# Kernel tuning notes

Hardware: AMD Instinct MI355X
Metric: run time of the kernel (lower is better)

The kernel has to match this reference:

```python
import jax, jax.numpy as jnp
import numpy as np

# Model/config constants (match init_kwargs)
B, S, D, H = 2, 2048, 512, 8
HD = D // H            # head dim = 64
WIN, DIL, G = 16, 2, 64  # window size, dilation rate, num global tokens
L = S - G              # 1984 local tokens (global indices are 0..G-1)


def setup_inputs() -> dict:
    key = jax.random.key(0)
    ks = jax.random.split(key, 16)
    sc = 0.02
    n = jax.random.normal
    return {
        "query": n(ks[0], (B, S, D), jnp.float32),
        "key": n(ks[1], (B, S, D), jnp.float32),
        "value": n(ks[2], (B, S, D), jnp.float32),
        # local multi-head attention params (linear_query/key/value/out_proj)
        "wq": n(ks[3], (D, D), jnp.float32) * sc, "bq": jnp.zeros((D,), jnp.float32),
        "wk": n(ks[4], (D, D), jnp.float32) * sc, "bk": jnp.zeros((D,), jnp.float32),
        "wv": n(ks[5], (D, D), jnp.float32) * sc, "bv": jnp.zeros((D,), jnp.float32),
        "wo": n(ks[6], (D, D), jnp.float32) * sc, "bo": jnp.zeros((D,), jnp.float32),
        # global nn.MultiheadAttention params (packed in_proj + out_proj)
        "g_in_w": n(ks[7], (3 * D, D), jnp.float32) * sc,
        "g_in_b": jnp.zeros((3 * D,), jnp.float32),
        "g_out_w": n(ks[8], (D, D), jnp.float32) * sc,
        "g_out_b": jnp.zeros((D,), jnp.float32),
    }


def _window_indices():
    # centered dilated window per local position, clipped to valid range
    pos = jnp.arange(L)
    offs = DIL * (jnp.arange(WIN) - WIN // 2)
    return jnp.clip(pos[:, None] + offs[None, :], 0, L - 1)


def reference(query, key, value, wq, bq, wk, bk, wv, bv, wo, bo,
              g_in_w, g_in_b, g_out_w, g_out_b):
    scale = 1.0 / np.sqrt(HD).astype(np.float32)

    # ---- local (dilated sliding window) path over tokens G..S-1 ----
    q_loc = query[:, G:, :]                      # (B, L, D)
    widx = _window_indices()
    k_win = key[:, G:, :][:, widx, :]
    v_win = value[:, G:, :][:, widx, :]

    q = (q_loc @ wq.T + bq).reshape(B, L, H, HD)          # (B,L,H,HD)
    k = (k_win @ wk.T + bk).reshape(B, L, WIN, H, HD)     # (B,L,W,H,HD)
    v = (v_win @ wv.T + bv).reshape(B, L, WIN, H, HD)

    scores = jnp.einsum('blhd,blwhd->blhw', q, k) * scale
    p = jax.nn.softmax(scores, axis=-1)
    o = jnp.einsum('blhw,blwhd->blhd', p, v).reshape(B, L, D)
    local_out = o @ wo.T + bo                              # (B,L,D)

    # ---- global token path: standard MHA over the G global tokens ----
    wq_g, wk_g, wv_g = g_in_w[:D], g_in_w[D:2 * D], g_in_w[2 * D:]
    bq_g, bk_g, bv_g = g_in_b[:D], g_in_b[D:2 * D], g_in_b[2 * D:]
    qg = (query[:, :G] @ wq_g.T + bq_g).reshape(B, G, H, HD)
    kg = (key[:, :G] @ wk_g.T + bk_g).reshape(B, G, H, HD)
    vg = (value[:, :G] @ wv_g.T + bv_g).reshape(B, G, H, HD)
    sg = jnp.einsum('bqhd,bkhd->bhqk', qg, kg) * scale     # (B,H,G,G)
    pg = jax.nn.softmax(sg, axis=-1)
    og = jnp.einsum('bhqk,bkhd->bqhd', pg, vg).reshape(B, G, D)
    global_out = og @ g_out_w.T + g_out_b                  # (B,G,D)

    # ---- fuse: scatter local + global back into full sequence ----
    out = jnp.zeros((B, S, D), query.dtype)
    out = out.at[:, G:, :].set(local_out)
    out = out.at[:, :G, :].set(global_out)
    return out
```

## Files before the change

### kernel.cpp

```cpp
#include <hip/hip_runtime.h>
#include <stdint.h>

#define B_ 2
#define S_ 2048
#define D_ 512
#define H_ 8
#define WIN_ 16
#define DIL_ 2
#define G_ 64
#define L_ (S_ - G_)

typedef short bf16x8 __attribute__((ext_vector_type(8)));
typedef float f32x4 __attribute__((ext_vector_type(4)));
typedef unsigned short u16;

__device__ __forceinline__ float bf2f(u16 h) {
  return __uint_as_float(((uint32_t)h) << 16);
}
__device__ __forceinline__ u16 f2bf(float f) {
  uint32_t u = __float_as_uint(f);
  uint32_t r = (u + 0x7fffu + ((u >> 16) & 1u)) >> 16;
  return (u16)r;
}

__device__ __forceinline__ void gload16(const u16* g, u16* l) {
  __builtin_amdgcn_global_load_lds(
      (const __attribute__((address_space(1))) void*)g,
      (__attribute__((address_space(3))) void*)l, 16, 0, 0);
}

struct CvtJob { const float* src; u16* dst; int n4; };
struct CvtArgs { CvtJob job[9]; };

__global__ __launch_bounds__(256) void cvt_kernel(CvtArgs a) {
  CvtJob j = a.job[blockIdx.y];
  int stride = gridDim.x * blockDim.x;
  for (int i = blockIdx.x * blockDim.x + threadIdx.x; i < j.n4; i += stride) {
    float4 v = reinterpret_cast<const float4*>(j.src)[i];
    ushort4 o;
    o.x = f2bf(v.x); o.y = f2bf(v.y); o.z = f2bf(v.z); o.w = f2bf(v.w);
    reinterpret_cast<ushort4*>(j.dst)[i] = o;
  }
}

struct Job {
  const u16* X; const u16* W; const float* bias; void* Y;
  int rpb;
  int xoff;
  long xbs;
  int yoff;
  long ybs;
  int out_f32;
};
struct GemmLaunch { int start[6]; Job job[6]; };

__global__ __launch_bounds__(256) void gemm_kernel(GemmLaunch a) {
  int bid = (int)blockIdx.x;
  bid = (bid & 7) * ((int)gridDim.x >> 3) + (bid >> 3);

  int j = 0;
#pragma unroll
  for (int i = 1; i < 6; ++i) j = (bid >= a.start[i]) ? i : j;
  const Job jb = a.job[j];
  bid -= a.start[j];
  const int tm = bid >> 2, tn = bid & 3;
  const int row0 = tm * 128, n0 = tn * 128;

  __shared__ __align__(16) u16 As[2][128 * 32];
  __shared__ __align__(16) u16 Bs[2][128 * 32];

  const int tid = threadIdx.x, lane = tid & 63, w = tid >> 6;
  const int wm = w >> 1, wn = w & 1;

  const int rA = tid >> 2;
  const int kq = (tid & 3) * 8;

  const int r0 = row0 + rA,      b0 = r0 >= jb.rpb;
  const int r1 = row0 + 64 + rA, b1 = r1 >= jb.rpb;
  const u16* xa0 = jb.X + (size_t)(b0 ? jb.xbs : 0) +
                   (size_t)(jb.xoff + r0 - (b0 ? jb.rpb : 0)) * 512 + kq;
  const u16* xa1 = jb.X + (size_t)(b1 ? jb.xbs : 0) +
                   (size_t)(jb.xoff + r1 - (b1 ? jb.rpb : 0)) * 512 + kq;
  const u16* wb0 = jb.W + (size_t)(n0 + rA) * 512 + kq;
  const u16* wb1 = jb.W + (size_t)(n0 + 64 + rA) * 512 + kq;

  f32x4 acc[4][4];
#pragma unroll
  for (int i = 0; i < 4; ++i)
#pragma unroll
    for (int k = 0; k < 4; ++k) acc[i][k] = (f32x4){0.f, 0.f, 0.f, 0.f};

  auto stage = [&](int buf, int kof) {
    gload16(xa0 + kof, &As[buf][w * 512]);
    gload16(xa1 + kof, &As[buf][2048 + w * 512]);
    gload16(wb0 + kof, &Bs[buf][w * 512]);
    gload16(wb1 + kof, &Bs[buf][2048 + w * 512]);
  };
  auto compute = [&](int buf) {
    bf16x8 af[4], bfv[4];
#pragma unroll
    for (int fm = 0; fm < 4; ++fm)
      af[fm] = *(const bf16x8*)&As[buf][(wm * 64 + fm * 16 + (lane & 15)) * 32 + 8 * (lane >> 4)];
#pragma unroll
    for (int fn = 0; fn < 4; ++fn)
      bfv[fn] = *(const bf16x8*)&Bs[buf][(wn * 64 + fn * 16 + (lane & 15)) * 32 + 8 * (lane >> 4)];
#pragma unroll
    for (int fm = 0; fm < 4; ++fm)
#pragma unroll
      for (int fn = 0; fn < 4; ++fn)
        acc[fm][fn] = __builtin_amdgcn_mfma_f32_16x16x32_bf16(af[fm], bfv[fn], acc[fm][fn], 0, 0, 0);
  };

  stage(0, 0);
  __syncthreads();
  int cur = 0;
  for (int kt = 0; kt < 15; ++kt) {
    stage(cur ^ 1, (kt + 1) * 32);
    compute(cur);
    __syncthreads();
    cur ^= 1;
  }
  compute(cur);

#pragma unroll
  for (int fm = 0; fm < 4; ++fm) {
#pragma unroll
    for (int fn = 0; fn < 4; ++fn) {
#pragma unroll
      for (int r = 0; r < 4; ++r) {
        const int row = row0 + wm * 64 + fm * 16 + (lane >> 4) * 4 + r;
        const int col = n0 + wn * 64 + fn * 16 + (lane & 15);
        const int b = row >= jb.rpb;
        const int rr = row - (b ? jb.rpb : 0);
        const size_t yi = (size_t)(b ? jb.ybs : 0) + (size_t)(jb.yoff + rr) * 512 + col;
        const float v = acc[fm][fn][r] + jb.bias[col];
        if (jb.out_f32) ((float*)jb.Y)[yi] = v;
        else            ((u16*)jb.Y)[yi]   = f2bf(v);
      }
    }
  }
}

__global__ __launch_bounds__(256) void attn_kernel(const u16* qp, const u16* kp,
                                                   const u16* vp, u16* ob,
                                                   const u16* qgp, const u16* kgp,
                                                   const u16* vgp, u16* ogp) {
  const int lane = threadIdx.x & 63;
  int bid = (int)blockIdx.x;
  const int nbl = (B_ * L_) / 4;
  if (bid < nbl) bid = (bid & 7) * (nbl >> 3) + (bid >> 3);
  const int wid = bid * 4 + (threadIdx.x >> 6);

  if (wid < B_ * L_) {
    const int l = wid % L_;
    const int brow = wid - l;
    float q[8];
    {
      bf16x8 qv = *(const bf16x8*)&qp[(size_t)wid * 512 + lane * 8];
#pragma unroll
      for (int e = 0; e < 8; ++e) q[e] = bf2f((u16)qv[e]);
    }
    float s[WIN_];
#pragma unroll
    for (int w2 = 0; w2 < WIN_; ++w2) {
      int ki = l + DIL_ * w2 - WIN_;
      ki = ki < 0 ? 0 : (ki > L_ - 1 ? L_ - 1 : ki);
      bf16x8 kv = *(const bf16x8*)&kp[(size_t)(brow + ki) * 512 + lane * 8];
      float p = 0.f;
#pragma unroll
      for (int e = 0; e < 8; ++e) p = fmaf(q[e], bf2f((u16)kv[e]), p);
      p += __shfl_xor(p, 1); p += __shfl_xor(p, 2); p += __shfl_xor(p, 4);
      s[w2] = p * 0.125f;
    }
    float m = s[0];
#pragma unroll
    for (int w2 = 1; w2 < WIN_; ++w2) m = fmaxf(m, s[w2]);
    float sum = 0.f;
#pragma unroll
    for (int w2 = 0; w2 < WIN_; ++w2) { s[w2] = __expf(s[w2] - m); sum += s[w2]; }
    const float inv = 1.0f / sum;
    float acc[8] = {0.f};
#pragma unroll
    for (int w2 = 0; w2 < WIN_; ++w2) {
      int ki = l + DIL_ * w2 - WIN_;
      ki = ki < 0 ? 0 : (ki > L_ - 1 ? L_ - 1 : ki);
      bf16x8 vv = *(const bf16x8*)&vp[(size_t)(brow + ki) * 512 + lane * 8];
#pragma unroll
      for (int e = 0; e < 8; ++e) acc[e] = fmaf(s[w2], bf2f((u16)vv[e]), acc[e]);
    }
    bf16x8 o8;
#pragma unroll
    for (int e = 0; e < 8; ++e) o8[e] = (short)f2bf(acc[e] * inv);
    *(bf16x8*)&ob[(size_t)wid * 512 + lane * 8] = o8;
  } else {
    const int g = wid - B_ * L_;
    const int base = (g >> 6) * 64;
    const int qi = g & 63;
    float q[8];
    {
      bf16x8 qv = *(const bf16x8*)&qgp[(size_t)(base + qi) * 512 + lane * 8];
#pragma unroll
      for (int e = 0; e < 8; ++e) q[e] = bf2f((u16)qv[e]);
    }
    float m = -1e30f, sum = 0.f, acc[8] = {0.f};
    for (int j2 = 0; j2 < 64; ++j2) {
      bf16x8 kv = *(const bf16x8*)&kgp[(size_t)(base + j2) * 512 + lane * 8];
      float p = 0.f;
#pragma unroll
      for (int e = 0; e < 8; ++e) p = fmaf(q[e], bf2f((u16)kv[e]), p);
      p += __shfl_xor(p, 1); p += __shfl_xor(p, 2); p += __shfl_xor(p, 4);
      p *= 0.125f;
      const float mn = fmaxf(m, p);
      const float c  = __expf(m - mn);
      const float pe = __expf(p - mn);
      sum = sum * c + pe;
      m = mn;
      bf16x8 vv = *(const bf16x8*)&vgp[(size_t)(base + j2) * 512 + lane * 8];
#pragma unroll
      for (int e = 0; e < 8; ++e) acc[e] = acc[e] * c + pe * bf2f((u16)vv[e]);
    }
    const float inv = 1.0f / sum;
    bf16x8 o8;
#pragma unroll
    for (int e = 0; e < 8; ++e) o8[e] = (short)f2bf(acc[e] * inv);
    *(bf16x8*)&ogp[(size_t)(base + qi) * 512 + lane * 8] = o8;
  }
}

extern "C" void kernel_launch(void* const* d_in, const int* in_sizes, int n_in,
                              void* d_out, int out_size, void* d_ws, size_t ws_size,
                              hipStream_t stream) {
  const float* query   = (const float*)d_in[0];
  const float* key     = (const float*)d_in[1];
  const float* value   = (const float*)d_in[2];
  const float* wq      = (const float*)d_in[3];
  const float* bq      = (const float*)d_in[4];
  const float* wk      = (const float*)d_in[5];
  const float* bk      = (const float*)d_in[6];
  const float* wv      = (const float*)d_in[7];
  const float* bv      = (const float*)d_in[8];
  const float* wo      = (const float*)d_in[9];
  const float* bo      = (const float*)d_in[10];
  const float* g_in_w  = (const float*)d_in[11];
  const float* g_in_b  = (const float*)d_in[12];
  const float* g_out_w = (const float*)d_in[13];
  const float* g_out_b = (const float*)d_in[14];
  float* out = (float*)d_out;

  u16* w16 = (u16*)d_ws;
  const size_t QKV = (size_t)B_ * S_ * D_;
  const size_t WSZ = (size_t)D_ * D_;
  const size_t PSZ = (size_t)B_ * L_ * D_;
  const size_t GSZ = (size_t)B_ * G_ * D_;

  u16* qb  = w16;              u16* kb  = qb + QKV;   u16* vb  = kb + QKV;
  u16* wqb = vb + QKV;         u16* wkb = wqb + WSZ;  u16* wvb = wkb + WSZ;
  u16* wob = wvb + WSZ;
  u16* gqw = wob + WSZ;        u16* gkw = gqw + WSZ;  u16* gvw = gkw + WSZ;
  u16* gow = gvw + WSZ;
  u16* qp  = gow + WSZ;        u16* kp  = qp + PSZ;   u16* vp  = kp + PSZ;
  u16* ob  = vp + PSZ;
  u16* qgp = ob + PSZ;         u16* kgp = qgp + GSZ;  u16* vgp = kgp + GSZ;
  u16* ogp = vgp + GSZ;

  CvtArgs ca;
  ca.job[0] = {query, qb, (int)(QKV / 4)};
  ca.job[1] = {key,   kb, (int)(QKV / 4)};
  ca.job[2] = {value, vb, (int)(QKV / 4)};
  ca.job[3] = {wq, wqb, (int)(WSZ / 4)};
  ca.job[4] = {wk, wkb, (int)(WSZ / 4)};
  ca.job[5] = {wv, wvb, (int)(WSZ / 4)};
  ca.job[6] = {wo, wob, (int)(WSZ / 4)};
  ca.job[7] = {g_in_w, gqw, (int)(3 * WSZ / 4)};
  ca.job[8] = {g_out_w, gow, (int)(WSZ / 4)};
  hipLaunchKernelGGL(cvt_kernel, dim3(512, 9), dim3(256), 0, stream, ca);

  const long XBS = (long)S_ * D_;
  const long PBS = (long)L_ * D_;
  const long GBS = (long)G_ * D_;

  GemmLaunch gi;
  gi.start[0] = 0; gi.start[1] = 124; gi.start[2] = 248;
  gi.start[3] = 372; gi.start[4] = 376; gi.start[5] = 380;
  gi.job[0] = {qb, wqb, bq, qp, L_, G_, XBS, 0, PBS, 0};
  gi.job[1] = {kb, wkb, bk, kp, L_, G_, XBS, 0, PBS, 0};
  gi.job[2] = {vb, wvb, bv, vp, L_, G_, XBS, 0, PBS, 0};
  gi.job[3] = {qb, gqw, g_in_b,           qgp, G_, 0, XBS, 0, GBS, 0};
  gi.job[4] = {kb, gkw, g_in_b + D_,      kgp, G_, 0, XBS, 0, GBS, 0};
  gi.job[5] = {vb, gvw, g_in_b + 2 * D_,  vgp, G_, 0, XBS, 0, GBS, 0};
  hipLaunchKernelGGL(gemm_kernel, dim3(384), dim3(256), 0, stream, gi);

  hipLaunchKernelGGL(attn_kernel, dim3((B_ * L_ + 128) / 4), dim3(256), 0, stream,
                     qp, kp, vp, ob, qgp, kgp, vgp, ogp);

  GemmLaunch go;
  go.start[0] = 0; go.start[1] = 124;
  go.start[2] = go.start[3] = go.start[4] = go.start[5] = 0x7fffffff;
  go.job[0] = {ob,  wob, bo,      out, L_, 0, PBS, G_, XBS, 1};
  go.job[1] = {ogp, gow, g_out_b, out, G_, 0, GBS, 0,  XBS, 1};
  go.job[2] = go.job[1]; go.job[3] = go.job[1]; go.job[4] = go.job[1]; go.job[5] = go.job[1];
  hipLaunchKernelGGL(gemm_kernel, dim3(128), dim3(256), 0, stream, go);
}
```

Measured before the change: 181.6 us.

## Fuse fp32-to-bf16 conversion into GEMM staging and drop separate convert kernel

Removes the standalone cvt_kernel, which converted all inputs and weights to bf16 in a separate pass. The GEMM now reads fp32 activations and weights directly, converts them in registers and stores bf16 to padded LDS. The padding (row stride 36) is meant to reduce bank conflicts. The tile changes to 128x64 to double the block count, and the async global_load_lds path is replaced by synchronous register loads, which costs memory-latency hiding and makes each weight tile be reconverted by many blocks.

```diff
diff --git a/kernel.cpp b/kernel.cpp
--- a/kernel.cpp
+++ b/kernel.cpp
@@ -14,6 +14,8 @@
 typedef float f32x4 __attribute__((ext_vector_type(4)));
 typedef unsigned short u16;
 
+#define LDSW 36
+
 __device__ __forceinline__ float bf2f(u16 h) {
   return __uint_as_float(((uint32_t)h) << 16);
 }
@@ -22,29 +24,12 @@
   uint32_t r = (u + 0x7fffu + ((u >> 16) & 1u)) >> 16;
   return (u16)r;
 }
-
-__device__ __forceinline__ void gload16(const u16* g, u16* l) {
-  __builtin_amdgcn_global_load_lds(
-      (const __attribute__((address_space(1))) void*)g,
-      (__attribute__((address_space(3))) void*)l, 16, 0, 0);
-}
-
-struct CvtJob { const float* src; u16* dst; int n4; };
-struct CvtArgs { CvtJob job[9]; };
-
-__global__ __launch_bounds__(256) void cvt_kernel(CvtArgs a) {
-  CvtJob j = a.job[blockIdx.y];
-  int stride = gridDim.x * blockDim.x;
-  for (int i = blockIdx.x * blockDim.x + threadIdx.x; i < j.n4; i += stride) {
-    float4 v = reinterpret_cast<const float4*>(j.src)[i];
-    ushort4 o;
-    o.x = f2bf(v.x); o.y = f2bf(v.y); o.z = f2bf(v.z); o.w = f2bf(v.w);
-    reinterpret_cast<ushort4*>(j.dst)[i] = o;
-  }
+__device__ __forceinline__ uint32_t pack2(float lo, float hi) {
+  return (uint32_t)f2bf(lo) | ((uint32_t)f2bf(hi) << 16);
 }
 
 struct Job {
-  const u16* X; const u16* W; const float* bias; void* Y;
+  const void* X; const float* W; const float* bias; void* Y;
   int rpb;
   int xoff;
   long xbs;
@@ -54,6 +39,7 @@
 };
 struct GemmLaunch { int start[6]; Job job[6]; };
 
+template <int X_BF16>
 __global__ __launch_bounds__(256) void gemm_kernel(GemmLaunch a) {
   int bid = (int)blockIdx.x;
   bid = (bid & 7) * ((int)gridDim.x >> 3) + (bid >> 3);
@@ -63,51 +49,66 @@
   for (int i = 1; i < 6; ++i) j = (bid >= a.start[i]) ? i : j;
   const Job jb = a.job[j];
   bid -= a.start[j];
-  const int tm = bid >> 2, tn = bid & 3;
-  const int row0 = tm * 128, n0 = tn * 128;
-
-  __shared__ __align__(16) u16 As[2][128 * 32];
-  __shared__ __align__(16) u16 Bs[2][128 * 32];
+  const int tm = bid >> 3, tn = bid & 7;
+  const int row0 = tm * 128, n0 = tn * 64;
+
+  __shared__ __align__(16) u16 As[2][128 * LDSW];
+  __shared__ __align__(16) u16 Bs[2][64 * LDSW];
 
   const int tid = threadIdx.x, lane = tid & 63, w = tid >> 6;
   const int wm = w >> 1, wn = w & 1;
 
-  const int rA = tid >> 2;
+  const int rs = tid >> 2;
   const int kq = (tid & 3) * 8;
 
-  const int r0 = row0 + rA,      b0 = r0 >= jb.rpb;
-  const int r1 = row0 + 64 + rA, b1 = r1 >= jb.rpb;
-  const u16* xa0 = jb.X + (size_t)(b0 ? jb.xbs : 0) +
-                   (size_t)(jb.xoff + r0 - (b0 ? jb.rpb : 0)) * 512 + kq;
-  const u16* xa1 = jb.X + (size_t)(b1 ? jb.xbs : 0) +
-                   (size_t)(jb.xoff + r1 - (b1 ? jb.rpb : 0)) * 512 + kq;
-  const u16* wb0 = jb.W + (size_t)(n0 + rA) * 512 + kq;
-  const u16* wb1 = jb.W + (size_t)(n0 + 64 + rA) * 512 + kq;
-
-  f32x4 acc[4][4];
+  const int r0 = row0 + rs,      b0 = r0 >= jb.rpb;
+  const int r1 = row0 + 64 + rs, b1 = r1 >= jb.rpb;
+  const size_t xi0 = (size_t)(b0 ? jb.xbs : 0) +
+                     (size_t)(jb.xoff + r0 - (b0 ? jb.rpb : 0)) * 512 + kq;
+  const size_t xi1 = (size_t)(b1 ? jb.xbs : 0) +
+                     (size_t)(jb.xoff + r1 - (b1 ? jb.rpb : 0)) * 512 + kq;
+  const float* wb0 = jb.W + (size_t)(n0 + rs) * 512 + kq;
+
+  f32x4 acc[4][2];
 #pragma unroll
   for (int i = 0; i < 4; ++i)
 #pragma unroll
-    for (int k = 0; k < 4; ++k) acc[i][k] = (f32x4){0.f, 0.f, 0.f, 0.f};
-
+    for (int k = 0; k < 2; ++k) acc[i][k] = (f32x4){0.f, 0.f, 0.f, 0.f};
+
+  auto cvt_store_f32 = [&](const float* src, u16* dst) {
+    float4 lo = *(const float4*)src;
+    float4 hi = *(const float4*)(src + 4);
+    int4 p;
+    p.x = (int)pack2(lo.x, lo.y);
+    p.y = (int)pack2(lo.z, lo.w);
+    p.z = (int)pack2(hi.x, hi.y);
+    p.w = (int)pack2(hi.z, hi.w);
+    *(int4*)dst = p;
+  };
   auto stage = [&](int buf, int kof) {
-    gload16(xa0 + kof, &As[buf][w * 512]);
-    gload16(xa1 + kof, &As[buf][2048 + w * 512]);
-    gload16(wb0 + kof, &Bs[buf][w * 512]);
-    gload16(wb1 + kof, &Bs[buf][2048 + w * 512]);
+    if (X_BF16) {
+      const u16* xb = (const u16*)jb.X;
+      *(int4*)&As[buf][rs * LDSW + kq]        = *(const int4*)&xb[xi0 + kof];
+      *(int4*)&As[buf][(64 + rs) * LDSW + kq] = *(const int4*)&xb[xi1 + kof];
+    } else {
+      const float* xf = (const float*)jb.X;
+      cvt_store_f32(xf + xi0 + kof, &As[buf][rs * LDSW + kq]);
+      cvt_store_f32(xf + xi1 + kof, &As[buf][(64 + rs) * LDSW + kq]);
+    }
+    cvt_store_f32(wb0 + kof, &Bs[buf][rs * LDSW + kq]);
   };
   auto compute = [&](int buf) {
-    bf16x8 af[4], bfv[4];
+    bf16x8 af[4], bfv[2];
 #pragma unroll
     for (int fm = 0; fm < 4; ++fm)
-      af[fm] = *(const bf16x8*)&As[buf][(wm * 64 + fm * 16 + (lane & 15)) * 32 + 8 * (lane >> 4)];
-#pragma unroll
-    for (int fn = 0; fn < 4; ++fn)
-      bfv[fn] = *(const bf16x8*)&Bs[buf][(wn * 64 + fn * 16 + (lane & 15)) * 32 + 8 * (lane >> 4)];
+      af[fm] = *(const bf16x8*)&As[buf][(wm * 64 + fm * 16 + (lane & 15)) * LDSW + 8 * (lane >> 4)];
+#pragma unroll
+    for (int fn = 0; fn < 2; ++fn)
+      bfv[fn] = *(const bf16x8*)&Bs[buf][(wn * 32 + fn * 16 + (lane & 15)) * LDSW + 8 * (lane >> 4)];
 #pragma unroll
     for (int fm = 0; fm < 4; ++fm)
 #pragma unroll
-      for (int fn = 0; fn < 4; ++fn)
+      for (int fn = 0; fn < 2; ++fn)
         acc[fm][fn] = __builtin_amdgcn_mfma_f32_16x16x32_bf16(af[fm], bfv[fn], acc[fm][fn], 0, 0, 0);
   };
 
@@ -125,11 +126,11 @@
 #pragma unroll
   for (int fm = 0; fm < 4; ++fm) {
 #pragma unroll
-    for (int fn = 0; fn < 4; ++fn) {
+    for (int fn = 0; fn < 2; ++fn) {
 #pragma unroll
       for (int r = 0; r < 4; ++r) {
         const int row = row0 + wm * 64 + fm * 16 + (lane >> 4) * 4 + r;
-        const int col = n0 + wn * 64 + fn * 16 + (lane & 15);
+        const int col = n0 + wn * 32 + fn * 16 + (lane & 15);
         const int b = row >= jb.rpb;
         const int rr = row - (b ? jb.rpb : 0);
         const size_t yi = (size_t)(b ? jb.ybs : 0) + (size_t)(jb.yoff + rr) * 512 + col;
@@ -248,56 +249,37 @@
   float* out = (float*)d_out;
 
   u16* w16 = (u16*)d_ws;
-  const size_t QKV = (size_t)B_ * S_ * D_;
-  const size_t WSZ = (size_t)D_ * D_;
   const size_t PSZ = (size_t)B_ * L_ * D_;
   const size_t GSZ = (size_t)B_ * G_ * D_;
 
-  u16* qb  = w16;              u16* kb  = qb + QKV;   u16* vb  = kb + QKV;
-  u16* wqb = vb + QKV;         u16* wkb = wqb + WSZ;  u16* wvb = wkb + WSZ;
-  u16* wob = wvb + WSZ;
-  u16* gqw = wob + WSZ;        u16* gkw = gqw + WSZ;  u16* gvw = gkw + WSZ;
-  u16* gow = gvw + WSZ;
-  u16* qp  = gow + WSZ;        u16* kp  = qp + PSZ;   u16* vp  = kp + PSZ;
+  u16* qp  = w16;        u16* kp  = qp + PSZ;   u16* vp  = kp + PSZ;
   u16* ob  = vp + PSZ;
-  u16* qgp = ob + PSZ;         u16* kgp = qgp + GSZ;  u16* vgp = kgp + GSZ;
+  u16* qgp = ob + PSZ;   u16* kgp = qgp + GSZ;  u16* vgp = kgp + GSZ;
   u16* ogp = vgp + GSZ;
-
-  CvtArgs ca;
-  ca.job[0] = {query, qb, (int)(QKV / 4)};
-  ca.job[1] = {key,   kb, (int)(QKV / 4)};
-  ca.job[2] = {value, vb, (int)(QKV / 4)};
-  ca.job[3] = {wq, wqb, (int)(WSZ / 4)};
-  ca.job[4] = {wk, wkb, (int)(WSZ / 4)};
-  ca.job[5] = {wv, wvb, (int)(WSZ / 4)};
-  ca.job[6] = {wo, wob, (int)(WSZ / 4)};
-  ca.job[7] = {g_in_w, gqw, (int)(3 * WSZ / 4)};
-  ca.job[8] = {g_out_w, gow, (int)(WSZ / 4)};
-  hipLaunchKernelGGL(cvt_kernel, dim3(512, 9), dim3(256), 0, stream, ca);
 
   const long XBS = (long)S_ * D_;
   const long PBS = (long)L_ * D_;
   const long GBS = (long)G_ * D_;
 
   GemmLaunch gi;
-  gi.start[0] = 0; gi.start[1] = 124; gi.start[2] = 248;
-  gi.start[3] = 372; gi.start[4] = 376; gi.start[5] = 380;
-  gi.job[0] = {qb, wqb, bq, qp, L_, G_, XBS, 0, PBS, 0};
-  gi.job[1] = {kb, wkb, bk, kp, L_, G_, XBS, 0, PBS, 0};
-  gi.job[2] = {vb, wvb, bv, vp, L_, G_, XBS, 0, PBS, 0};
-  gi.job[3] = {qb, gqw, g_in_b,           qgp, G_, 0, XBS, 0, GBS, 0};
-  gi.job[4] = {kb, gkw, g_in_b + D_,      kgp, G_, 0, XBS, 0, GBS, 0};
-  gi.job[5] = {vb, gvw, g_in_b + 2 * D_,  vgp, G_, 0, XBS, 0, GBS, 0};
-  hipLaunchKernelGGL(gemm_kernel, dim3(384), dim3(256), 0, stream, gi);
+  gi.start[0] = 0; gi.start[1] = 248; gi.start[2] = 496;
+  gi.start[3] = 744; gi.start[4] = 752; gi.start[5] = 760;
+  gi.job[0] = {query, wq, bq, qp, L_, G_, XBS, 0, PBS, 0};
+  gi.job[1] = {key,   wk, bk, kp, L_, G_, XBS, 0, PBS, 0};
+  gi.job[2] = {value, wv, bv, vp, L_, G_, XBS, 0, PBS, 0};
+  gi.job[3] = {query, g_in_w,             g_in_b,          qgp, G_, 0, XBS, 0, GBS, 0};
+  gi.job[4] = {key,   g_in_w + 512 * D_,  g_in_b + D_,     kgp, G_, 0, XBS, 0, GBS, 0};
+  gi.job[5] = {value, g_in_w + 1024 * D_, g_in_b + 2 * D_, vgp, G_, 0, XBS, 0, GBS, 0};
+  hipLaunchKernelGGL(gemm_kernel<0>, dim3(768), dim3(256), 0, stream, gi);
 
   hipLaunchKernelGGL(attn_kernel, dim3((B_ * L_ + 128) / 4), dim3(256), 0, stream,
                      qp, kp, vp, ob, qgp, kgp, vgp, ogp);
 
   GemmLaunch go;
-  go.start[0] = 0; go.start[1] = 124;
+  go.start[0] = 0; go.start[1] = 248;
   go.start[2] = go.start[3] = go.start[4] = go.start[5] = 0x7fffffff;
-  go.job[0] = {ob,  wob, bo,      out, L_, 0, PBS, G_, XBS, 1};
-  go.job[1] = {ogp, gow, g_out_b, out, G_, 0, GBS, 0,  XBS, 1};
+  go.job[0] = {ob,  wo,      bo,      out, L_, 0, PBS, G_, XBS, 1};
+  go.job[1] = {ogp, g_out_w, g_out_b, out, G_, 0, GBS, 0,  XBS, 1};
   go.job[2] = go.job[1]; go.job[3] = go.job[1]; go.job[4] = go.job[1]; go.job[5] = go.job[1];
-  hipLaunchKernelGGL(gemm_kernel, dim3(128), dim3(256), 0, stream, go);
-}
+  hipLaunchKernelGGL(gemm_kernel<1>, dim3(256), dim3(256), 0, stream, go);
+}
```

Measured after the change: 182.5 us. About the same (+0.5%).
